# Kernel tuning notes

Measured on AMD Instinct MI355X. Metric: run time of the kernel, lower is better.

Reference implementation:

```python
import jax, jax.numpy as jnp
import numpy as np

NUM_HEADS = 16
HEAD_DIM = 128
POLY_ORDER = 4
LRPE_BASE = 10000.0
EPS = 1e-6


def _rope(x, offset=0):
    # x: [b, n, h, d] -- Lrpe type-1 rotary position embedding per head dim
    d = x.shape[-1]
    half = d // 2
    theta = LRPE_BASE ** (-jnp.arange(half, dtype=jnp.float32) * 2.0 / d)  # [half]
    pos = jnp.arange(x.shape[1], dtype=jnp.float32) + offset               # [n]
    ang = pos[:, None] * theta[None, :]                                    # [n, half]
    cos = jnp.cos(ang)[None, :, None, :]
    sin = jnp.sin(ang)[None, :, None, :]
    x1, x2 = x[..., :half], x[..., half:]
    return jnp.concatenate([x1 * cos - x2 * sin, x1 * sin + x2 * cos], axis=-1)


def setup_inputs() -> dict:
    key = jax.random.key(0)
    ks = jax.random.split(key, 5)
    b, n, d = 2, 2048, 2048
    std = 0.02  # init_std from module
    x = jax.random.normal(ks[0], (b, n, d), dtype=jnp.float32)
    Wq = jax.random.normal(ks[1], (d, d), dtype=jnp.float32) * std
    Wk = jax.random.normal(ks[2], (d, d), dtype=jnp.float32) * std
    Wv = jax.random.normal(ks[3], (d, d), dtype=jnp.float32) * std
    Wo = jax.random.normal(ks[4], (d, d), dtype=jnp.float32) * std
    return {"x": x, "Wq": Wq, "Wk": Wk, "Wv": Wv, "Wo": Wo}


def reference(x, Wq, Wk, Wv, Wo):
    b, n, d = x.shape
    h, hd = NUM_HEADS, HEAD_DIM
    # projections (nn.Linear: x @ W.T)
    q = (x @ Wq.T).reshape(b, n, h, hd)
    k = (x @ Wk.T).reshape(b, n, h, hd)
    v = (x @ Wv.T).reshape(b, n, h, hd)
    # LRPE (rotary, type 1), offset = 0 (no cache)
    q = _rope(q)
    k = _rope(k)
    # polynomial (non-softmax) attention: scores = (q.k)^p, causal mask,
    # row-normalized (linear-attention-style denominator)
    scores = jnp.einsum("bnhd,bmhd->bhnm", q, k) ** POLY_ORDER  # p=4 even -> >=0
    causal = jnp.tril(jnp.ones((n, n), dtype=scores.dtype))
    scores = scores * causal
    denom = jnp.maximum(scores.sum(-1, keepdims=True), EPS)      # [b,h,n,1]
    out = jnp.einsum("bhnm,bmhd->bhnd", scores, v) / denom        # [b,h,n,hd]
    out = out.transpose(0, 2, 1, 3).reshape(b, n, d)              # b n (h d)
    return out @ Wo.T
```

## Files before the change

kernel.cpp:

```cpp
#include <hip/hip_runtime.h>


typedef __bf16 bf16;
typedef __bf16 bf16x8 __attribute__((ext_vector_type(8)));
typedef __bf16 bf16x4 __attribute__((ext_vector_type(4)));
typedef float f32x4 __attribute__((ext_vector_type(4)));

#define GLD(g, l)                                                   \
  __builtin_amdgcn_global_load_lds(                                 \
      (const __attribute__((address_space(1))) void*)(g),           \
      (__attribute__((address_space(3))) void*)(l), 16, 0, 0)

#define MFMA(a, b, c) __builtin_amdgcn_mfma_f32_16x16x32_bf16(a, b, c, 0, 0, 0)

__global__ __launch_bounds__(256) void k_cvt(const float* __restrict__ in,
                                             bf16* __restrict__ out, int n4) {
  int i = blockIdx.x * 256 + threadIdx.x;
  if (i >= n4) return;
  float4 v = reinterpret_cast<const float4*>(in)[i];
  bf16x4 o = {(bf16)v.x, (bf16)v.y, (bf16)v.z, (bf16)v.w};
  reinterpret_cast<bf16x4*>(out)[i] = o;
}

__global__ __launch_bounds__(256) void k_cvt3(const float* __restrict__ a,
                                              const float* __restrict__ b,
                                              const float* __restrict__ c,
                                              bf16* __restrict__ out) {
  int i = blockIdx.x * 256 + threadIdx.x;
  const float* src = (i < 1048576) ? a : ((i < 2097152) ? b : c);
  int off = i & 1048575;
  float4 v = reinterpret_cast<const float4*>(src)[off];
  bf16x4 o = {(bf16)v.x, (bf16)v.y, (bf16)v.z, (bf16)v.w};
  reinterpret_cast<bf16x4*>(out)[i] = o;
}

__global__ __launch_bounds__(256) void k_rope_tab(float* __restrict__ ct,
                                                  float* __restrict__ st) {
  int i = blockIdx.x * 256 + threadIdx.x;
  if (i >= 2048 * 64) return;
  int pos = i >> 6, f = i & 63;
  float theta = exp2f(-(float)f * 0.20762050593046014f);
  float ang = (float)pos * theta;
  ct[i] = cosf(ang);
  st[i] = sinf(ang);
}

__global__ __launch_bounds__(256, 2) void k_gemm_qkv(
    const bf16* __restrict__ Am, const bf16* __restrict__ Bm,
    bf16* __restrict__ Qp, bf16* __restrict__ Kp, bf16* __restrict__ Vt,
    const float* __restrict__ ct, const float* __restrict__ st) {
  __shared__ __align__(16) char LDS[73728];
  const int tid = threadIdx.x, w = tid >> 6, l = tid & 63;
  const int lr = l & 15, g = l >> 4;
  const int wr = w >> 1, wc = w & 1;
  const int tm = blockIdx.y * 256, tn = blockIdx.x * 128;

  const int rl = tid >> 2;
  const int scol = (((tid & 3) ^ (rl & 3) ^ ((rl >> 2) & 3)) << 3);
  const int xo = ((g ^ (lr & 3) ^ ((lr >> 2) & 3)) << 4);

#define STAGEQ(buf, kt)                                                      \
  {                                                                          \
    _Pragma("unroll") for (int i = 0; i < 4; ++i)                            \
        GLD(Am + (size_t)(tm + i * 64 + rl) * 2048 + (kt) + scol,            \
            LDS + (buf) * 24576 + i * 4096 + tid * 16);                      \
    _Pragma("unroll") for (int i = 0; i < 2; ++i)                            \
        GLD(Bm + (size_t)(tn + i * 64 + rl) * 2048 + (kt) + scol,            \
            LDS + (buf) * 24576 + 16384 + i * 4096 + tid * 16);              \
  }

  f32x4 acc[8][4] = {};

  STAGEQ(0, 0);
  STAGEQ(1, 32);
  int cur = 0, st3 = 2;
  for (int t = 0; t < 63; ++t) {
    asm volatile("s_waitcnt vmcnt(6)" ::: "memory");
    __builtin_amdgcn_s_barrier();
    asm volatile("" ::: "memory");
    if (t < 62) STAGEQ(st3, (t + 2) * 32);
    const char* pa = LDS + cur * 24576;
    const char* pb = pa + 16384;
    bf16x8 a[8], b[4];
#pragma unroll
    for (int fm = 0; fm < 8; ++fm)
      a[fm] = *reinterpret_cast<const bf16x8*>(pa + (wr * 128 + fm * 16 + lr) * 64 + xo);
#pragma unroll
    for (int nf = 0; nf < 4; ++nf)
      b[nf] = *reinterpret_cast<const bf16x8*>(pb + (wc * 64 + nf * 16 + lr) * 64 + xo);
    __builtin_amdgcn_s_setprio(1);
#pragma unroll
    for (int fm = 0; fm < 8; ++fm)
#pragma unroll
      for (int nf = 0; nf < 4; ++nf)
        acc[fm][nf] = MFMA(a[fm], b[nf], acc[fm][nf]);
    __builtin_amdgcn_s_setprio(0);
    cur = (cur == 2) ? 0 : cur + 1;
    st3 = (st3 == 2) ? 0 : st3 + 1;
  }
  {
    asm volatile("s_waitcnt vmcnt(0)" ::: "memory");
    __builtin_amdgcn_s_barrier();
    asm volatile("" ::: "memory");
    const char* pa = LDS + cur * 24576;
    const char* pb = pa + 16384;
    bf16x8 a[8], b[4];
#pragma unroll
    for (int fm = 0; fm < 8; ++fm)
      a[fm] = *reinterpret_cast<const bf16x8*>(pa + (wr * 128 + fm * 16 + lr) * 64 + xo);
#pragma unroll
    for (int nf = 0; nf < 4; ++nf)
      b[nf] = *reinterpret_cast<const bf16x8*>(pb + (wc * 64 + nf * 16 + lr) * 64 + xo);
#pragma unroll
    for (int fm = 0; fm < 8; ++fm)
#pragma unroll
      for (int nf = 0; nf < 4; ++nf)
        acc[fm][nf] = MFMA(a[fm], b[nf], acc[fm][nf]);
  }

  if (tn < 4096) {
    __syncthreads();
    bf16* E = (bf16*)LDS;
#pragma unroll
    for (int fm = 0; fm < 8; ++fm)
#pragma unroll
      for (int nf = 0; nf < 4; ++nf)
#pragma unroll
        for (int rr = 0; rr < 4; ++rr)
          E[(wr * 128 + fm * 16 + g * 4 + rr) * 136 + wc * 64 + nf * 16 + lr] =
              (bf16)acc[fm][nf][rr];
    __syncthreads();
    const int hh = (tn & 2047) >> 7;
    bf16* dst = (tn < 2048) ? Qp : Kp;
#pragma unroll
    for (int i = 0; i < 16; ++i) {
      int task = i * 256 + tid;
      int row = task >> 4, dg = (task & 15) << 2;
      int token = tm + row, nn = token & 2047, bb = token >> 11;
      f32x4 c4 = *reinterpret_cast<const f32x4*>(ct + nn * 64 + dg);
      f32x4 s4 = *reinterpret_cast<const f32x4*>(st + nn * 64 + dg);
      bf16x4 x1 = *reinterpret_cast<const bf16x4*>(E + row * 136 + dg);
      bf16x4 x2 = *reinterpret_cast<const bf16x4*>(E + row * 136 + 64 + dg);
      bf16x4 o1, o2;
#pragma unroll
      for (int j = 0; j < 4; ++j) {
        float a1 = (float)x1[j], a2 = (float)x2[j];
        o1[j] = (bf16)(a1 * c4[j] - a2 * s4[j]);
        o2[j] = (bf16)(a1 * s4[j] + a2 * c4[j]);
      }
      size_t rb = (((size_t)bb * 16 + hh) * 2048 + nn) * 128;
      *reinterpret_cast<bf16x4*>(dst + rb + dg) = o1;
      *reinterpret_cast<bf16x4*>(dst + rb + 64 + dg) = o2;
    }
  } else {
#pragma unroll
    for (int fm = 0; fm < 8; ++fm)
#pragma unroll
      for (int nf = 0; nf < 4; ++nf) {
        int row0 = tm + wr * 128 + fm * 16 + g * 4;
        int col = (tn - 4096) + wc * 64 + nf * 16 + lr;
        int bb = row0 >> 11, nn = row0 & 2047;
        int hh = col >> 7, dd = col & 127;
        bf16x4 o = {(bf16)acc[fm][nf][0], (bf16)acc[fm][nf][1],
                    (bf16)acc[fm][nf][2], (bf16)acc[fm][nf][3]};
        *reinterpret_cast<bf16x4*>(
            Vt + (((size_t)bb * 16 + hh) * 128 + dd) * 2048 + nn) = o;
      }
  }
}

__global__ __launch_bounds__(256, 3) void k_gemm_out(const bf16* __restrict__ Am,
                                                     const bf16* __restrict__ Bm,
                                                     float* __restrict__ C) {
  __shared__ __align__(16) char LDS[49152];
  const int tid = threadIdx.x, w = tid >> 6, l = tid & 63;
  const int lr = l & 15, g = l >> 4;
  const int wr = w >> 1, wc = w & 1;
  const int tm = blockIdx.y * 128, tn = blockIdx.x * 128;

  const int rl = tid >> 2;
  const int scol = (((tid & 3) ^ (rl & 3) ^ ((rl >> 2) & 3)) << 3);
  const int xo = ((g ^ (lr & 3) ^ ((lr >> 2) & 3)) << 4);

#define STAGEO(buf, kt)                                                      \
  {                                                                          \
    _Pragma("unroll") for (int i = 0; i < 2; ++i)                            \
        GLD(Am + (size_t)(tm + i * 64 + rl) * 2048 + (kt) + scol,            \
            LDS + (buf) * 16384 + i * 4096 + tid * 16);                      \
    _Pragma("unroll") for (int i = 0; i < 2; ++i)                            \
        GLD(Bm + (size_t)(tn + i * 64 + rl) * 2048 + (kt) + scol,            \
            LDS + (buf) * 16384 + 8192 + i * 4096 + tid * 16);               \
  }

  f32x4 acc[4][4] = {};

  STAGEO(0, 0);
  STAGEO(1, 32);
  int cur = 0, st3 = 2;
  for (int t = 0; t < 63; ++t) {
    asm volatile("s_waitcnt vmcnt(4)" ::: "memory");
    __builtin_amdgcn_s_barrier();
    asm volatile("" ::: "memory");
    if (t < 62) STAGEO(st3, (t + 2) * 32);
    const char* pa = LDS + cur * 16384;
    const char* pb = pa + 8192;
    bf16x8 a[4], b[4];
#pragma unroll
    for (int fm = 0; fm < 4; ++fm)
      a[fm] = *reinterpret_cast<const bf16x8*>(pa + (wr * 64 + fm * 16 + lr) * 64 + xo);
#pragma unroll
    for (int nf = 0; nf < 4; ++nf)
      b[nf] = *reinterpret_cast<const bf16x8*>(pb + (wc * 64 + nf * 16 + lr) * 64 + xo);
    __builtin_amdgcn_s_setprio(1);
#pragma unroll
    for (int fm = 0; fm < 4; ++fm)
#pragma unroll
      for (int nf = 0; nf < 4; ++nf)
        acc[fm][nf] = MFMA(a[fm], b[nf], acc[fm][nf]);
    __builtin_amdgcn_s_setprio(0);
    cur = (cur == 2) ? 0 : cur + 1;
    st3 = (st3 == 2) ? 0 : st3 + 1;
  }
  {
    asm volatile("s_waitcnt vmcnt(0)" ::: "memory");
    __builtin_amdgcn_s_barrier();
    asm volatile("" ::: "memory");
    const char* pa = LDS + cur * 16384;
    const char* pb = pa + 8192;
    bf16x8 a[4], b[4];
#pragma unroll
    for (int fm = 0; fm < 4; ++fm)
      a[fm] = *reinterpret_cast<const bf16x8*>(pa + (wr * 64 + fm * 16 + lr) * 64 + xo);
#pragma unroll
    for (int nf = 0; nf < 4; ++nf)
      b[nf] = *reinterpret_cast<const bf16x8*>(pb + (wc * 64 + nf * 16 + lr) * 64 + xo);
#pragma unroll
    for (int fm = 0; fm < 4; ++fm)
#pragma unroll
      for (int nf = 0; nf < 4; ++nf)
        acc[fm][nf] = MFMA(a[fm], b[nf], acc[fm][nf]);
  }

#pragma unroll
  for (int fm = 0; fm < 4; ++fm)
#pragma unroll
    for (int nf = 0; nf < 4; ++nf)
#pragma unroll
      for (int rr = 0; rr < 4; ++rr) {
        int row = tm + wr * 64 + fm * 16 + g * 4 + rr;
        int col = tn + wc * 64 + nf * 16 + lr;
        C[(size_t)row * 2048 + col] = acc[fm][nf][rr];
      }
}

__global__ __launch_bounds__(256) void k_attn(const bf16* __restrict__ Q,
                                              const bf16* __restrict__ K,
                                              const bf16* __restrict__ Vt,
                                              bf16* __restrict__ O) {
  __shared__ __align__(16) bf16 Ks[128 * 128];
  __shared__ __align__(16) bf16 Vs[128 * 128];
  __shared__ __align__(16) bf16 Ps[64 * 128];
  const int tid = threadIdx.x, w = tid >> 6, l = tid & 63;
  const int lr = l & 15, g = l >> 4;
  const int flat = blockIdx.x;
  const int pair = flat >> 5, bh = flat & 31;
  const size_t base = (size_t)bh * 2048 * 128;
  const int b_ = bh >> 4, h_ = bh & 15;

  bf16x8 vones = {};
  if (lr == 0) {
#pragma unroll
    for (int j = 0; j < 8; ++j) vones[j] = (bf16)1.0f;
  }

  for (int seg = 0; seg < 2; ++seg) {
    const int qt = seg ? (31 - pair) : pair;
    const int qbase = qt * 64;
    bf16x8 qf[4];
#pragma unroll
    for (int kc = 0; kc < 4; ++kc)
      qf[kc] = *reinterpret_cast<const bf16x8*>(
          Q + base + (size_t)(qbase + w * 16 + lr) * 128 + kc * 32 + g * 8);

    f32x4 on[8] = {};
    f32x4 dn4 = {0.f, 0.f, 0.f, 0.f};
    const int nt = (qbase >> 7) + 1;

    for (int t = 0; t < nt; ++t) {
      const bf16* kg = K + base + (size_t)t * 128 * 128;
      const bf16* vg = Vt + base + t * 128;
#pragma unroll
      for (int r = 0; r < 8; ++r) {
        int e = r * 2048 + w * 512 + l * 8;
        int row = e >> 7, c = (e >> 3) & 15;
        int sc = ((c ^ (row & 7)) << 3);
        GLD(kg + (row << 7) + sc, Ks + r * 2048 + w * 512);
        GLD(vg + (size_t)row * 2048 + sc, Vs + r * 2048 + w * 512);
      }
      __syncthreads();

      f32x4 s[8] = {};
      __builtin_amdgcn_s_setprio(1);
#pragma unroll
      for (int kc = 0; kc < 4; ++kc)
#pragma unroll
        for (int ni = 0; ni < 8; ++ni) {
          bf16x8 kb = *reinterpret_cast<const bf16x8*>(
              Ks + ((ni * 16 + lr) << 7) + (((kc * 4 + g) ^ (lr & 7)) << 3));
          s[ni] = MFMA(qf[kc], kb, s[ni]);
        }
      __builtin_amdgcn_s_setprio(0);

      const bool diag = (t == nt - 1);
#pragma unroll
      for (int ni = 0; ni < 8; ++ni)
#pragma unroll
        for (int r = 0; r < 4; ++r) {
          int lrow = g * 4 + r;
          float v = s[ni][r];
          if (diag) {
            int qrow = qbase + w * 16 + lrow;
            int col = t * 128 + ni * 16 + lr;
            v = (col <= qrow) ? v : 0.f;
          }
          float v2 = v * v, v4 = v2 * v2;
          int chunk = ni * 2 + (lr >> 3);
          Ps[((w * 16 + lrow) << 7) + ((chunk ^ (lrow & 7)) << 3) + (lr & 7)] =
              (bf16)v4;
        }

      __builtin_amdgcn_s_setprio(1);
#pragma unroll
      for (int kc = 0; kc < 4; ++kc) {
        bf16x8 pa = *reinterpret_cast<const bf16x8*>(
            Ps + ((w * 16 + lr) << 7) + (((kc * 4 + g) ^ (lr & 7)) << 3));
        dn4 = MFMA(pa, vones, dn4);
#pragma unroll
        for (int ni = 0; ni < 8; ++ni) {
          bf16x8 vb = *reinterpret_cast<const bf16x8*>(
              Vs + ((ni * 16 + lr) << 7) + (((kc * 4 + g) ^ (lr & 7)) << 3));
          on[ni] = MFMA(pa, vb, on[ni]);
        }
      }
      __builtin_amdgcn_s_setprio(0);
      __syncthreads();
    }

#pragma unroll
    for (int r = 0; r < 4; ++r) {
      float d = __shfl(dn4[r], l & 48);
      float inv = 1.0f / fmaxf(d, 1e-6f);
      int row = qbase + w * 16 + g * 4 + r;
#pragma unroll
      for (int ni = 0; ni < 8; ++ni)
        O[((size_t)b_ * 2048 + row) * 2048 + h_ * 128 + ni * 16 + lr] =
            (bf16)(on[ni][r] * inv);
    }
  }
}

extern "C" void kernel_launch(void* const* d_in, const int* in_sizes, int n_in,
                              void* d_out, int out_size, void* d_ws, size_t ws_size,
                              hipStream_t stream) {
  const float* x  = (const float*)d_in[0];
  const float* Wq = (const float*)d_in[1];
  const float* Wk = (const float*)d_in[2];
  const float* Wv = (const float*)d_in[3];
  const float* Wo = (const float*)d_in[4];
  float* out = (float*)d_out;

  char* p = (char*)d_ws;
  bf16* xb   = (bf16*)p; p += (size_t)8388608 * 2;
  bf16* wqkv = (bf16*)p; p += (size_t)12582912 * 2;
  bf16* wob  = (bf16*)p; p += (size_t)4194304 * 2;
  bf16* Qp   = (bf16*)p; p += (size_t)8388608 * 2;
  bf16* Kp   = (bf16*)p; p += (size_t)8388608 * 2;
  bf16* Vt   = (bf16*)p; p += (size_t)8388608 * 2;
  bf16* Ob   = (bf16*)p; p += (size_t)8388608 * 2;
  float* ct  = (float*)p; p += (size_t)131072 * 4;
  float* st  = (float*)p; p += (size_t)131072 * 4;

  k_cvt<<<8192, 256, 0, stream>>>(x, xb, 2097152);
  k_cvt3<<<12288, 256, 0, stream>>>(Wq, Wk, Wv, wqkv);
  k_cvt<<<4096, 256, 0, stream>>>(Wo, wob, 1048576);
  k_rope_tab<<<512, 256, 0, stream>>>(ct, st);

  k_gemm_qkv<<<dim3(48, 16), 256, 0, stream>>>(xb, wqkv, Qp, Kp, Vt, ct, st);

  k_attn<<<512, 256, 0, stream>>>(Qp, Kp, Vt, Ob);

  k_gemm_out<<<dim3(16, 32), 256, 0, stream>>>(Ob, wob, out);
}
```

Measured before the change: 271.4 us.

## Double-buffer K tiles in LDS and stream V directly into registers

```diff
diff --git a/kernel.cpp b/kernel.cpp
--- a/kernel.cpp
+++ b/kernel.cpp
@@ -257,8 +257,7 @@
                                               const bf16* __restrict__ K,
                                               const bf16* __restrict__ Vt,
                                               bf16* __restrict__ O) {
-  __shared__ __align__(16) bf16 Ks[128 * 128];
-  __shared__ __align__(16) bf16 Vs[128 * 128];
+  __shared__ __align__(16) bf16 Ks[2][128 * 128];
   __shared__ __align__(16) bf16 Ps[64 * 128];
   const int tid = threadIdx.x, w = tid >> 6, l = tid & 63;
   const int lr = l & 15, g = l >> 4;
@@ -273,6 +272,17 @@
     for (int j = 0; j < 8; ++j) vones[j] = (bf16)1.0f;
   }
 
+#define STAGEK(tt, buf)                                              \
+  {                                                                  \
+    const bf16* kg = K + base + (size_t)(tt) * 128 * 128;            \
+    _Pragma("unroll") for (int r = 0; r < 8; ++r) {                  \
+      int e = r * 2048 + w * 512 + l * 8;                            \
+      int row = e >> 7, cc = (e >> 3) & 15;                          \
+      GLD(kg + (row << 7) + (((cc ^ (row & 7))) << 3),               \
+          Ks[buf] + r * 2048 + w * 512);                             \
+    }                                                                \
+  }
+
   for (int seg = 0; seg < 2; ++seg) {
     const int qt = seg ? (31 - pair) : pair;
     const int qbase = qt * 64;
@@ -286,19 +296,25 @@
     f32x4 dn4 = {0.f, 0.f, 0.f, 0.f};
     const int nt = (qbase >> 7) + 1;
 
+    __builtin_amdgcn_s_barrier();
+    STAGEK(0, 0);
+
     for (int t = 0; t < nt; ++t) {
-      const bf16* kg = K + base + (size_t)t * 128 * 128;
-      const bf16* vg = Vt + base + t * 128;
-#pragma unroll
-      for (int r = 0; r < 8; ++r) {
-        int e = r * 2048 + w * 512 + l * 8;
-        int row = e >> 7, c = (e >> 3) & 15;
-        int sc = ((c ^ (row & 7)) << 3);
-        GLD(kg + (row << 7) + sc, Ks + r * 2048 + w * 512);
-        GLD(vg + (size_t)row * 2048 + sc, Vs + r * 2048 + w * 512);
-      }
-      __syncthreads();
-
+      bf16x8 vb[4][8];
+#pragma unroll
+      for (int kc = 0; kc < 4; ++kc)
+#pragma unroll
+        for (int ni = 0; ni < 8; ++ni)
+          vb[kc][ni] = *reinterpret_cast<const bf16x8*>(
+              Vt + base + (size_t)(ni * 16 + lr) * 2048 + t * 128 + kc * 32 + g * 8);
+
+      __builtin_amdgcn_s_barrier();
+      int tn1 = (t + 1 < nt) ? t + 1 : nt - 1;
+      STAGEK(tn1, (t + 1) & 1);
+      asm volatile("s_waitcnt vmcnt(40)" ::: "memory");
+      __builtin_amdgcn_s_barrier();
+
+      const bf16* kcur = Ks[t & 1];
       f32x4 s[8] = {};
       __builtin_amdgcn_s_setprio(1);
 #pragma unroll
@@ -306,7 +322,7 @@
 #pragma unroll
         for (int ni = 0; ni < 8; ++ni) {
           bf16x8 kb = *reinterpret_cast<const bf16x8*>(
-              Ks + ((ni * 16 + lr) << 7) + (((kc * 4 + g) ^ (lr & 7)) << 3));
+              kcur + ((ni * 16 + lr) << 7) + (((kc * 4 + g) ^ (lr & 7)) << 3));
           s[ni] = MFMA(qf[kc], kb, s[ni]);
         }
       __builtin_amdgcn_s_setprio(0);
@@ -329,6 +345,8 @@
               (bf16)v4;
         }
 
+      asm volatile("s_waitcnt vmcnt(8)" ::: "memory");
+
       __builtin_amdgcn_s_setprio(1);
 #pragma unroll
       for (int kc = 0; kc < 4; ++kc) {
@@ -336,14 +354,10 @@
             Ps + ((w * 16 + lr) << 7) + (((kc * 4 + g) ^ (lr & 7)) << 3));
         dn4 = MFMA(pa, vones, dn4);
 #pragma unroll
-        for (int ni = 0; ni < 8; ++ni) {
-          bf16x8 vb = *reinterpret_cast<const bf16x8*>(
-              Vs + ((ni * 16 + lr) << 7) + (((kc * 4 + g) ^ (lr & 7)) << 3));
-          on[ni] = MFMA(pa, vb, on[ni]);
-        }
+        for (int ni = 0; ni < 8; ++ni)
+          on[ni] = MFMA(pa, vb[kc][ni], on[ni]);
       }
       __builtin_amdgcn_s_setprio(0);
-      __syncthreads();
     }
 
 #pragma unroll
@@ -357,6 +371,7 @@
             (bf16)(on[ni][r] * inv);
     }
   }
+#undef STAGEK
 }
 
 extern "C" void kernel_launch(void* const* d_in, const int* in_sizes, int n_in,
```

After: 366.9 us. 1.35x slower.
